# Kernel optimization log

Hardware: AMD Instinct MI355X
Metric: run time of the kernel (lower is better)

## Reference

```python
import jax, jax.numpy as jnp
import numpy as np

B, C, K, P, STRIDE, ITERS = 32, 32, 3, 4, 1, 3
PSIZE = P * P
EPS = 1e-6


def unfold_patches(x, K, stride):
    # Replicates F.unfold(x_chw, kernel_size=K, padding=K//2, stride=stride)
    # followed by transpose(1,2).view(b, oh, ow, K*K, c) — including the
    # channel-major flat ordering that the view reinterprets.
    b, h, w, c = x.shape
    pad = K // 2
    xp = jnp.pad(jnp.transpose(x, (0, 3, 1, 2)), ((0, 0), (0, 0), (pad, pad), (pad, pad)))
    oh = (h + 2 * pad - K) // stride + 1
    ow = (w + 2 * pad - K) // stride + 1
    rows = []
    for ki in range(K):
        cols = []
        for kj in range(K):
            cols.append(xp[:, :, ki:ki + (oh - 1) * stride + 1:stride, kj:kj + (ow - 1) * stride + 1:stride])
        rows.append(jnp.stack(cols, axis=2))  # (b, c, K, oh, ow)
    pat = jnp.stack(rows, axis=2)  # (b, c, K, K, oh, ow)
    pat = pat.reshape(b, c * K * K, oh * ow)  # unfold output (b, c*K*K, L)
    pat = jnp.transpose(pat, (0, 2, 1)).reshape(b, oh, ow, K * K, c)
    return pat, oh, ow


def squash(s, eps=EPS):
    s2 = jnp.sum(s * s, axis=-1, keepdims=True)
    return (s2 / (1.0 + s2)) * s / jnp.sqrt(s2 + eps)


def dynamic_routing(v, a_in, iters=ITERS, eps=EPS):
    # v: (n, in_votes, C, psize), a_in: (n, in_votes, 1)
    n, in_votes, Cc, _ = v.shape
    b_ij = jnp.zeros((n, in_votes, Cc), dtype=v.dtype)
    a_in = jnp.clip(a_in, 0.0001, 1.0)
    v_j = None
    for t in range(iters):
        c_ij = jax.nn.softmax(b_ij, axis=2) * a_in
        c_ij = c_ij / (jnp.sum(c_ij, axis=2, keepdims=True) + eps)
        s_j = jnp.einsum('nic,nicq->ncq', c_ij, v)
        v_j = squash(s_j)
        if t < iters - 1:
            agreement = jnp.einsum('nicq,ncq->nic', v, v_j)
            b_ij = b_ij + agreement
    a_out = jnp.clip(jnp.sqrt(jnp.sum(v_j * v_j, axis=-1) + eps), 0.0001, 1.0 - 0.0001)
    return v_j, a_out


def setup_inputs() -> dict:
    key = jax.random.key(0)
    k1, k2 = jax.random.split(key)
    x = jax.random.normal(k1, (2, 14, 14, B * (PSIZE + 1)), dtype=jnp.float32)
    weights = jax.random.normal(k2, (K * K * B, C, PSIZE, PSIZE), dtype=jnp.float32) * 0.02
    return {"x": x, "weights": weights}


def reference(x, weights):
    b, h, w, c = x.shape
    patches, oh, ow = unfold_patches(x, K, STRIDE)
    p_in = patches[..., :B * PSIZE].reshape(b * oh * ow, K * K * B, PSIZE)
    a_in = patches[..., B * PSIZE:].reshape(b * oh * ow, K * K * B, 1)
    votes = jnp.einsum('bip,icpq->bicq', p_in, weights)  # (n, KKB, C, psize)
    p_vec, a_vec = dynamic_routing(votes, a_in)
    p_out = p_vec.reshape(b, oh, ow, C * PSIZE)
    a_out = a_vec.reshape(b, oh, ow, C)
    out = jnp.concatenate([p_out, a_out], axis=3)
    p_out = jnp.nan_to_num(p_out, nan=0.0, posinf=10000.0, neginf=-10000.0)
    a_out = jnp.nan_to_num(a_out, nan=0.5, posinf=1.0 - 0.0001, neginf=0.0001)
    out = jnp.nan_to_num(out, nan=0.0, posinf=10000.0, neginf=-10000.0)
    return p_out, a_out, out
```

## Files before the change

### kernel.cpp

```cpp
#include <hip/hip_runtime.h>
#include <hip/hip_fp16.h>
#include <math.h>

#define NB 392
#define NI 288
#define NC 32
#define NQ 16
#define CQ 512
#define CH 544
#define EPSV 1e-6f

#define VSCALE 32.0f
#define VINV (1.0f / 32.0f)

#define OFF_AOUT 200704
#define OFF_CAT  213248

#define RT_THREADS 512
#define RT_WAVES 8

typedef _Float16 v4h __attribute__((ext_vector_type(4)));
typedef float v4f __attribute__((ext_vector_type(4)));
typedef float v2f __attribute__((ext_vector_type(2)));

__device__ __forceinline__ float gather_x(const float* __restrict__ x, int n, int j) {
    int c_idx = j / 9;
    int rem = j - c_idx * 9;
    int ki = rem / 3;
    int kj = rem - ki * 3;
    int b_ = n / 196;
    int rest = n - b_ * 196;
    int yy = rest / 14;
    int xx = rest - yy * 14;
    int iy = yy + ki - 1;
    int ix = xx + kj - 1;
    float v = 0.f;
    if ((unsigned)iy < 14u && (unsigned)ix < 14u)
        v = x[((b_ * 14 + iy) * 14 + ix) * CH + c_idx];
    return v;
}

__global__ __launch_bounds__(256) void votes_k(const float* __restrict__ x,
                                               const float* __restrict__ wts,
                                               uchar* __restrict__ votes) {
    __shared__ uint tile[64 * 36];
    int mtt = blockIdx.x;
    int i = blockIdx.y;
    int t = threadIdx.x;
    int wv = t >> 6;
    int l = t & 63;
    int col = l & 15;
    int quad = l >> 4;

    int n_row = mtt * 64 + wv * 16 + col;
    v4h av = {};
    if (n_row < NB) {
        int jb = (i >> 5) * CH + (i & 31) * 16 + quad * 4;
#pragma unroll
        for (int kk = 0; kk < 4; ++kk)
            av[kk] = (_Float16)gather_x(x, n_row, jb + kk);
    }

    const float* wb = wts + (size_t)i * 8192 + quad * 64 + col;
    const uchar* tileb = (const uchar*)tile;

    for (int ch = 0; ch < 4; ++ch) {
#pragma unroll
        for (int c8 = 0; c8 < 8; ++c8) {
            int ct = ch * 8 + c8;
            const float* wp = wb + ct * 256;
            v4h bv;
            bv[0] = (_Float16)wp[0];
            bv[1] = (_Float16)wp[16];
            bv[2] = (_Float16)wp[32];
            bv[3] = (_Float16)wp[48];
            v4f acc = {0.f, 0.f, 0.f, 0.f};
            acc = __builtin_amdgcn_mfma_f32_16x16x16f16(bv, av, acc, 0, 0, 0);
            uint u = __builtin_amdgcn_cvt_pk_fp8_f32(acc[0] * VSCALE, acc[1] * VSCALE, 0, false);
            u = __builtin_amdgcn_cvt_pk_fp8_f32(acc[2] * VSCALE, acc[3] * VSCALE, u, true);
            tile[(wv * 16 + col) * 36 + c8 * 4 + quad] = u;
        }
        __syncthreads();
#pragma unroll
        for (int k = 0; k < 2; ++k) {
            int idx = k * 256 + t;
            int row = idx >> 3;
            int off = idx & 7;
            int n_out = mtt * 64 + row;
            if (n_out < NB) {
                uint4 d = *(const uint4*)&tileb[row * 144 + off * 16];
                *(uint4*)(votes + (((size_t)n_out * NI + i) << 9) + ch * 128 + off * 16) = d;
            }
        }
        __syncthreads();
    }
}

__global__ __launch_bounds__(RT_THREADS) void routing_k(const uchar* __restrict__ votes,
                                                        const float* __restrict__ x,
                                                        float* __restrict__ out) {
    __shared__ float afs[NI];
    __shared__ float sred[RT_WAVES * CQ];
    __shared__ float vj[CQ];
    __shared__ float aout_s[NC];

    int n = blockIdx.x;
    int t = threadIdx.x;
    int wv = t >> 6;
    int l = t & 63;
    int c = l & 31;
    int g = l >> 5;

    if (t < NI) {
        int j = (t >> 5) * CH + 512 + (t & 31);
        float v = gather_x(x, n, j);
        float a = fminf(fmaxf(v, 1e-4f), 1.0f);
        afs[t] = a / (a + EPSV);
    }
    __syncthreads();

    const uchar* vb = votes + (size_t)n * NI * 512;
    float vjr[16];
    float sreg[16];

#define VROW(S) (((const uint4*)(vb + ((size_t)(((((S) << 3) + wv) << 1) + g) << 9)))[c])

    for (int iter = 0; iter < 3; ++iter) {
#pragma unroll
        for (int q = 0; q < 16; ++q) sreg[q] = 0.f;

        uint4 f0 = VROW(0), f1 = VROW(1), f2 = VROW(2), f3 = VROW(3);

#pragma clang loop unroll_count(2)
        for (int s = 0; s < 18; ++s) {
            int i = ((s << 3) + wv) * 2 + g;
            uint4 cur = f0;
            f0 = f1; f1 = f2; f2 = f3;
            if (s + 4 < 18) f3 = VROW(s + 4);

            float vt[16];
            {
                v2f p;
                p = __builtin_amdgcn_cvt_pk_f32_fp8(cur.x, false); vt[0] = p[0];  vt[1] = p[1];
                p = __builtin_amdgcn_cvt_pk_f32_fp8(cur.x, true);  vt[2] = p[0];  vt[3] = p[1];
                p = __builtin_amdgcn_cvt_pk_f32_fp8(cur.y, false); vt[4] = p[0];  vt[5] = p[1];
                p = __builtin_amdgcn_cvt_pk_f32_fp8(cur.y, true);  vt[6] = p[0];  vt[7] = p[1];
                p = __builtin_amdgcn_cvt_pk_f32_fp8(cur.z, false); vt[8] = p[0];  vt[9] = p[1];
                p = __builtin_amdgcn_cvt_pk_f32_fp8(cur.z, true);  vt[10] = p[0]; vt[11] = p[1];
                p = __builtin_amdgcn_cvt_pk_f32_fp8(cur.w, false); vt[12] = p[0]; vt[13] = p[1];
                p = __builtin_amdgcn_cvt_pk_f32_fp8(cur.w, true);  vt[14] = p[0]; vt[15] = p[1];
            }
            float cij;
            if (iter == 0) {
                cij = afs[i] * (1.0f / 32.0f);
            } else {
                float ah = 0.f;
#pragma unroll
                for (int q = 0; q < 16; ++q) ah += vt[q] * vjr[q];
                float e = __expf(ah);
                float ssum = e;
                ssum += __shfl_xor(ssum, 1);
                ssum += __shfl_xor(ssum, 2);
                ssum += __shfl_xor(ssum, 4);
                ssum += __shfl_xor(ssum, 8);
                ssum += __shfl_xor(ssum, 16);
                cij = e * __builtin_amdgcn_rcpf(ssum) * afs[i];
            }
#pragma unroll
            for (int q = 0; q < 16; ++q) sreg[q] += cij * vt[q];
        }

#pragma unroll
        for (int q = 0; q < 16; ++q) sreg[q] += __shfl_xor(sreg[q], 32);
        if (g == 0) {
            float* sw = &sred[wv * CQ + c];
#pragma unroll
            for (int q = 0; q < 16; ++q) sw[q * 32] = sreg[q];
        }
        __syncthreads();
        {
            float ssum = 0.f;
#pragma unroll
            for (int k = 0; k < RT_WAVES; ++k) ssum += sred[k * CQ + t];
            sred[t] = ssum * VINV;
        }
        __syncthreads();

        if (t < NC) {
            float s2 = 0.f;
#pragma unroll
            for (int q = 0; q < 16; ++q) {
                float s = sred[q * 32 + t];
                s2 += s * s;
            }
            float f = (s2 / (1.f + s2)) / sqrtf(s2 + EPSV);
            float vn2 = 0.f;
#pragma unroll
            for (int q = 0; q < 16; ++q) {
                float v = f * sred[q * 32 + t];
                vj[q * 32 + t] = v;
                vn2 += v * v;
            }
            if (iter == 2) {
                float ao = sqrtf(vn2 + EPSV);
                ao = fminf(fmaxf(ao, 1e-4f), 1.f - 1e-4f);
                aout_s[t] = ao;
            }
        }
        __syncthreads();
        if (iter < 2) {
#pragma unroll
            for (int q = 0; q < 16; ++q) {
                float v = vj[q * 32 + c] * VINV;
                vjr[q] = (iter == 0) ? v : vjr[q] + v;
            }
        }
    }

    {
        float v = vj[(t & 15) * 32 + (t >> 4)];
        out[(size_t)n * CQ + t] = v;
        out[OFF_CAT + (size_t)n * 544 + t] = v;
    }
    if (t < NC) {
        float ao = aout_s[t];
        out[OFF_AOUT + n * 32 + t] = ao;
        out[OFF_CAT + (size_t)n * 544 + 512 + t] = ao;
    }
}

extern "C" void kernel_launch(void* const* d_in, const int* in_sizes, int n_in,
                              void* d_out, int out_size, void* d_ws, size_t ws_size,
                              hipStream_t stream) {
    const float* x = (const float*)d_in[0];
    const float* wts = (const float*)d_in[1];
    float* out = (float*)d_out;
    uchar* votes = (uchar*)d_ws;

    hipLaunchKernelGGL(votes_k, dim3(7, NI), dim3(256), 0, stream,
                       x, wts, votes);
    hipLaunchKernelGGL(routing_k, dim3(NB), dim3(RT_THREADS), 0, stream,
                       votes, x, out);
}
```

Before: 115.2 us.

## Cache routing votes in LDS and reduce partial sums with shared atomics

The routing kernel now stages each block's fp8 votes (288x512 bytes) into shared memory during the first iteration. Later iterations read the votes from LDS instead of re-reading global memory. The cross-wave reduction buffer is replaced by atomicAdd into a single 512-float shared accumulator, which shrinks that buffer. The 144KB LDS footprint limits occupancy to one block per CU, and the shared atomics may contend.

After: 152.3 us. 1.32x slower.

```diff
diff --git a/kernel.cpp b/kernel.cpp
--- a/kernel.cpp
+++ b/kernel.cpp
@@ -99,8 +99,9 @@
 __global__ __launch_bounds__(RT_THREADS) void routing_k(const uchar* __restrict__ votes,
                                                         const float* __restrict__ x,
                                                         float* __restrict__ out) {
+    __shared__ uchar vlds[NI * 512];
     __shared__ float afs[NI];
-    __shared__ float sred[RT_WAVES * CQ];
+    __shared__ float sacc[CQ];
     __shared__ float vj[CQ];
     __shared__ float aout_s[NC];
 
@@ -117,7 +118,6 @@
         float a = fminf(fmaxf(v, 1e-4f), 1.0f);
         afs[t] = a / (a + EPSV);
     }
-    __syncthreads();
 
     const uchar* vb = votes + (size_t)n * NI * 512;
     float vjr[16];
@@ -126,34 +126,53 @@
 #define VROW(S) (((const uint4*)(vb + ((size_t)(((((S) << 3) + wv) << 1) + g) << 9)))[c])
 
     for (int iter = 0; iter < 3; ++iter) {
+        sacc[t] = 0.f;
+        __syncthreads();
 #pragma unroll
         for (int q = 0; q < 16; ++q) sreg[q] = 0.f;
 
-        uint4 f0 = VROW(0), f1 = VROW(1), f2 = VROW(2), f3 = VROW(3);
-
+        if (iter == 0) {
+            uint4 f0 = VROW(0), f1 = VROW(1), f2 = VROW(2), f3 = VROW(3);
 #pragma clang loop unroll_count(2)
-        for (int s = 0; s < 18; ++s) {
-            int i = ((s << 3) + wv) * 2 + g;
-            uint4 cur = f0;
-            f0 = f1; f1 = f2; f2 = f3;
-            if (s + 4 < 18) f3 = VROW(s + 4);
-
-            float vt[16];
-            {
-                v2f p;
-                p = __builtin_amdgcn_cvt_pk_f32_fp8(cur.x, false); vt[0] = p[0];  vt[1] = p[1];
-                p = __builtin_amdgcn_cvt_pk_f32_fp8(cur.x, true);  vt[2] = p[0];  vt[3] = p[1];
-                p = __builtin_amdgcn_cvt_pk_f32_fp8(cur.y, false); vt[4] = p[0];  vt[5] = p[1];
-                p = __builtin_amdgcn_cvt_pk_f32_fp8(cur.y, true);  vt[6] = p[0];  vt[7] = p[1];
-                p = __builtin_amdgcn_cvt_pk_f32_fp8(cur.z, false); vt[8] = p[0];  vt[9] = p[1];
-                p = __builtin_amdgcn_cvt_pk_f32_fp8(cur.z, true);  vt[10] = p[0]; vt[11] = p[1];
-                p = __builtin_amdgcn_cvt_pk_f32_fp8(cur.w, false); vt[12] = p[0]; vt[13] = p[1];
-                p = __builtin_amdgcn_cvt_pk_f32_fp8(cur.w, true);  vt[14] = p[0]; vt[15] = p[1];
-            }
-            float cij;
-            if (iter == 0) {
-                cij = afs[i] * (1.0f / 32.0f);
-            } else {
+            for (int s = 0; s < 18; ++s) {
+                int i = ((s << 3) + wv) * 2 + g;
+                uint4 cur = f0;
+                f0 = f1; f1 = f2; f2 = f3;
+                if (s + 4 < 18) f3 = VROW(s + 4);
+                *(uint4*)&vlds[i * 512 + c * 16] = cur;
+                float vt[16];
+                {
+                    v2f p;
+                    p = __builtin_amdgcn_cvt_pk_f32_fp8(cur.x, false); vt[0] = p[0];  vt[1] = p[1];
+                    p = __builtin_amdgcn_cvt_pk_f32_fp8(cur.x, true);  vt[2] = p[0];  vt[3] = p[1];
+                    p = __builtin_amdgcn_cvt_pk_f32_fp8(cur.y, false); vt[4] = p[0];  vt[5] = p[1];
+                    p = __builtin_amdgcn_cvt_pk_f32_fp8(cur.y, true);  vt[6] = p[0];  vt[7] = p[1];
+                    p = __builtin_amdgcn_cvt_pk_f32_fp8(cur.z, false); vt[8] = p[0];  vt[9] = p[1];
+                    p = __builtin_amdgcn_cvt_pk_f32_fp8(cur.z, true);  vt[10] = p[0]; vt[11] = p[1];
+                    p = __builtin_amdgcn_cvt_pk_f32_fp8(cur.w, false); vt[12] = p[0]; vt[13] = p[1];
+                    p = __builtin_amdgcn_cvt_pk_f32_fp8(cur.w, true);  vt[14] = p[0]; vt[15] = p[1];
+                }
+                float cij = afs[i] * (1.0f / 32.0f);
+#pragma unroll
+                for (int q = 0; q < 16; ++q) sreg[q] += cij * vt[q];
+            }
+        } else {
+#pragma clang loop unroll_count(2)
+            for (int s = 0; s < 18; ++s) {
+                int i = ((s << 3) + wv) * 2 + g;
+                uint4 cur = *(const uint4*)&vlds[i * 512 + c * 16];
+                float vt[16];
+                {
+                    v2f p;
+                    p = __builtin_amdgcn_cvt_pk_f32_fp8(cur.x, false); vt[0] = p[0];  vt[1] = p[1];
+                    p = __builtin_amdgcn_cvt_pk_f32_fp8(cur.x, true);  vt[2] = p[0];  vt[3] = p[1];
+                    p = __builtin_amdgcn_cvt_pk_f32_fp8(cur.y, false); vt[4] = p[0];  vt[5] = p[1];
+                    p = __builtin_amdgcn_cvt_pk_f32_fp8(cur.y, true);  vt[6] = p[0];  vt[7] = p[1];
+                    p = __builtin_amdgcn_cvt_pk_f32_fp8(cur.z, false); vt[8] = p[0];  vt[9] = p[1];
+                    p = __builtin_amdgcn_cvt_pk_f32_fp8(cur.z, true);  vt[10] = p[0]; vt[11] = p[1];
+                    p = __builtin_amdgcn_cvt_pk_f32_fp8(cur.w, false); vt[12] = p[0]; vt[13] = p[1];
+                    p = __builtin_amdgcn_cvt_pk_f32_fp8(cur.w, true);  vt[14] = p[0]; vt[15] = p[1];
+                }
                 float ah = 0.f;
 #pragma unroll
                 for (int q = 0; q < 16; ++q) ah += vt[q] * vjr[q];
@@ -164,40 +183,34 @@
                 ssum += __shfl_xor(ssum, 4);
                 ssum += __shfl_xor(ssum, 8);
                 ssum += __shfl_xor(ssum, 16);
-                cij = e * __builtin_amdgcn_rcpf(ssum) * afs[i];
-            }
-#pragma unroll
-            for (int q = 0; q < 16; ++q) sreg[q] += cij * vt[q];
+                float cij = e * __builtin_amdgcn_rcpf(ssum) * afs[i];
+#pragma unroll
+                for (int q = 0; q < 16; ++q) sreg[q] += cij * vt[q];
+            }
         }
 
 #pragma unroll
         for (int q = 0; q < 16; ++q) sreg[q] += __shfl_xor(sreg[q], 32);
         if (g == 0) {
-            float* sw = &sred[wv * CQ + c];
-#pragma unroll
-            for (int q = 0; q < 16; ++q) sw[q * 32] = sreg[q];
-        }
-        __syncthreads();
-        {
-            float ssum = 0.f;
-#pragma unroll
-            for (int k = 0; k < RT_WAVES; ++k) ssum += sred[k * CQ + t];
-            sred[t] = ssum * VINV;
+#pragma unroll
+            for (int q = 0; q < 16; ++q) atomicAdd(&sacc[q * 32 + c], sreg[q]);
         }
         __syncthreads();
 
         if (t < NC) {
             float s2 = 0.f;
+            float sv[16];
 #pragma unroll
             for (int q = 0; q < 16; ++q) {
-                float s = sred[q * 32 + t];
+                float s = sacc[q * 32 + t] * VINV;
+                sv[q] = s;
                 s2 += s * s;
             }
             float f = (s2 / (1.f + s2)) / sqrtf(s2 + EPSV);
             float vn2 = 0.f;
 #pragma unroll
             for (int q = 0; q < 16; ++q) {
-                float v = f * sred[q * 32 + t];
+                float v = f * sv[q];
                 vj[q * 32 + t] = v;
                 vn2 += v * v;
             }
```
